# Kernel optimization log

Hardware: AMD Instinct MI355X
Metric: run time of the kernel (lower is better)

Reference implementation:

```python
import jax, jax.numpy as jnp
import numpy as np

T, D, E, DE = 50000, 128, 1600000, 3
EPS = 1e-5


def setup_inputs() -> dict:
    key = jax.random.key(0)
    ks = jax.random.split(key, 8)
    H = jax.random.normal(ks[0], (T, D), dtype=jnp.float32)
    edge_index = jax.random.randint(ks[1], (2, E), 0, T, dtype=jnp.int64)
    edge_attr = jax.random.normal(ks[2], (E, DE), dtype=jnp.float32)
    # phi: Linear(D+DE -> D), GELU, Linear(D -> D)
    s1 = 1.0 / np.sqrt(D + DE)
    s2 = 1.0 / np.sqrt(D)
    W1 = jax.random.uniform(ks[3], (D + DE, D), minval=-s1, maxval=s1, dtype=jnp.float32)
    b1 = jax.random.uniform(ks[4], (D,), minval=-s1, maxval=s1, dtype=jnp.float32)
    W2 = jax.random.uniform(ks[5], (D, D), minval=-s2, maxval=s2, dtype=jnp.float32)
    b2 = jax.random.uniform(ks[6], (D,), minval=-s2, maxval=s2, dtype=jnp.float32)
    gamma = jnp.ones((D,), dtype=jnp.float32)
    beta = jnp.zeros((D,), dtype=jnp.float32)
    return {"H": H, "edge_index": edge_index, "edge_attr": edge_attr,
            "W1": W1, "b1": b1, "W2": W2, "b2": b2, "gamma": gamma, "beta": beta}


def reference(H, edge_index, edge_attr, W1, b1, W2, b2, gamma, beta):
    src, dst = edge_index[0], edge_index[1]
    Hj = H[src]                                   # [E, D] gather
    feat = jnp.concatenate([Hj, edge_attr], axis=-1)  # [E, D+DE]
    h = jax.nn.gelu(feat @ W1 + b1, approximate=False)
    m = h @ W2 + b2                               # [E, D] messages
    agg = jax.ops.segment_sum(m, dst, num_segments=H.shape[0])  # scatter-add
    x = H + agg
    mu = jnp.mean(x, axis=-1, keepdims=True)
    var = jnp.mean((x - mu) ** 2, axis=-1, keepdims=True)
    return (x - mu) * jax.lax.rsqrt(var + EPS) * gamma + beta
```

## Files before the change

kernel.cpp:

```cpp
#include <hip/hip_runtime.h>
#include <hip/hip_bf16.h>

typedef unsigned short u16;
typedef unsigned int u32;
typedef __attribute__((ext_vector_type(8))) __bf16 bf16x8;
typedef __attribute__((ext_vector_type(4))) float f32x4;

#define NT 50000
#define NEDGE 1600000
#define GRID 512
#define NWV 8
#define TOTW 4096
#define NBIN 50176

__device__ __forceinline__ u16 f2bf(float f) {
  unsigned x = __float_as_uint(f);
  x += 0x7fffu + ((x >> 16) & 1u);
  return (u16)(x >> 16);
}

__device__ __forceinline__ int swz(int row, int col) {
  return (row << 7) + (col ^ ((row & 7) << 3));
}

__device__ __forceinline__ float gelu(float v) {
  float t = v * (0.797884561f + 0.0356774081f * v * v);
  return v * __builtin_amdgcn_rcpf(1.0f + __expf(-2.0f * t));
}

__device__ __forceinline__ void atomAddF32(float* p, float v) {
#if defined(__has_builtin)
#if __has_builtin(__builtin_amdgcn_global_atomic_fadd_f32)
  __builtin_amdgcn_global_atomic_fadd_f32((__attribute__((address_space(1))) float*)p, v);
  return;
#endif
#endif
  atomicAdd(p, v);
}


__global__ void prep_all(const float* __restrict__ H, u16* __restrict__ Hb,
                         const float* __restrict__ W1, const float* __restrict__ W2,
                         u16* __restrict__ wsw, const float* __restrict__ b1,
                         u16* __restrict__ wx, u32* __restrict__ cnt) {
  int bid = blockIdx.x, tid = threadIdx.x;
  if (bid < 3125) {
    int t = bid * 256 + tid;
    const float4* s = (const float4*)H + (long)t * 2;
    float4 a = s[0], c = s[1];
    int4 pk;
    pk.x = f2bf(a.x) | ((int)f2bf(a.y) << 16);
    pk.y = f2bf(a.z) | ((int)f2bf(a.w) << 16);
    pk.z = f2bf(c.x) | ((int)f2bf(c.y) << 16);
    pk.w = f2bf(c.z) | ((int)f2bf(c.w) << 16);
    ((int4*)Hb)[t] = pk;
  } else if (bid < 3253) {
    int t = (bid - 3125) * 256 + tid;
    int m = t >> 14;
    int p = t & 16383;
    int row = p >> 7;
    int colq = p & 127;
    int k = colq ^ ((row & 7) << 3);
    const float* W = m ? W2 : W1;
    wsw[t] = f2bf(W[k * 128 + row]);
  } else if (bid < 3257) {
    int t = (bid - 3253) * 256 + tid;
    int row = t >> 3, j = t & 7;
    float v = 0.f;
    if (j < 3) v = W1[(128 + j) * 128 + row];
    else if (j == 3) v = b1[row];
    wx[t] = f2bf(v);
  } else if (bid < 3453) {
    int t = (bid - 3257) * 256 + tid;
    if (t < NBIN) cnt[t] = 0;
  } else {
    if (tid < 16) ((int4*)(Hb + (long)NT * 128))[tid] = make_int4(0, 0, 0, 0);
  }
}

__global__ void copy_h(const float4* __restrict__ H, float4* __restrict__ out) {
  int t = blockIdx.x * 256 + threadIdx.x;
  out[t] = H[t];
}


__global__ void hist_g(const int* __restrict__ ei, u32* __restrict__ cnt) {
  int e = blockIdx.x * 256 + threadIdx.x;
  atomicAdd(&cnt[ei[NEDGE + e]], 1u);
}

__global__ void scan_blk(u32* __restrict__ cnt, u32* __restrict__ btot) {
  __shared__ u32 ls[1024];
  int tid = threadIdx.x;
  int bin = blockIdx.x * 1024 + tid;
  u32 c = cnt[bin];
  ls[tid] = c;
  __syncthreads();
  for (int o = 1; o < 1024; o <<= 1) {
    u32 t = (tid >= o) ? ls[tid - o] : 0u;
    __syncthreads();
    ls[tid] += t;
    __syncthreads();
  }
  cnt[bin] = ls[tid] - c;
  if (tid == 1023) btot[blockIdx.x] = ls[1023];
}

__global__ void scan_btot(u32* __restrict__ btot) {
  if (threadIdx.x == 0) {
    u32 run = 0;
    for (int i = 0; i < 49; ++i) { u32 t = btot[i]; btot[i] = run; run += t; }
  }
}

__global__ void fin_base(const u32* __restrict__ cnt, const u32* __restrict__ btot,
                         u32* __restrict__ base, u32* __restrict__ pos) {
  int bin = blockIdx.x * 256 + threadIdx.x;
  if (bin < NT) {
    u32 v = cnt[bin] + btot[bin >> 10];
    base[bin] = v;
    pos[bin] = v;
  }
  if (bin == NT) base[NT] = NEDGE;
}

__global__ void scatter_g(const int* __restrict__ ei, const float* __restrict__ ea,
                          u32* __restrict__ pos, uint2* __restrict__ rec) {
  int e = blockIdx.x * 256 + threadIdx.x;
  int d = ei[NEDGE + e];
  int s = ei[e];
  float e0 = ea[e * 3 + 0], e1 = ea[e * 3 + 1], e2 = ea[e * 3 + 2];
  u32 p = atomicAdd(&pos[d], 1u);
  rec[p] = make_uint2((u32)s | ((u32)f2bf(e0) << 16),
                      (u32)f2bf(e1) | ((u32)f2bf(e2) << 16));
}


__launch_bounds__(512, 2)
__global__ void msg_agg(const u16* __restrict__ Hb,
                        const u16* __restrict__ wsw,
                        const u16* __restrict__ wx,
                        const u32* __restrict__ base,
                        const uint2* __restrict__ rec,
                        u16* __restrict__ hsb) {
  __shared__ __align__(16) u16 lw1[16384];
  __shared__ __align__(16) u16 lw1x[128 * 8];

  const int tid = threadIdx.x;
  {
    const int4* g = (const int4*)wsw;
    int4* d1 = (int4*)lw1;
#pragma unroll
    for (int i = 0; i < 4; ++i) { int c = tid + i * 512; d1[c] = g[c]; }
  }
  if (tid < 128) ((int4*)lw1x)[tid] = ((const int4*)wx)[tid];
  __syncthreads();

  const int wv = tid >> 6, lane = tid & 63;
  const int l15 = lane & 15, l4 = lane >> 4;

  const int gid = blockIdx.x * NWV + wv;
  const int d0 = (int)(((long)gid * NT) / TOTW);
  const int d1i = (int)(((long)(gid + 1) * NT) / TOTW);
  const int nd = d1i - d0;

  for (int b = 0; b < nd; ++b) {
    const int start = (int)base[d0 + b];
    const int cnt = (int)base[d0 + b + 1] - start;

    float racc[8][4];
#pragma unroll
    for (int nt = 0; nt < 8; ++nt)
#pragma unroll
      for (int r = 0; r < 4; ++r) racc[nt][r] = 0.f;

    const int ntile = (cnt + 15) >> 4;
    uint2 r2c = make_uint2(0, 0);
    if (ntile > 0) {
      int i0 = (l15 < cnt) ? l15 : cnt - 1;
      r2c = rec[start + i0];
    }

    for (int t = 0; t < ntile; ++t) {
      int inx = (t + 1) * 16 + l15;
      if (inx >= cnt) inx = cnt - 1;
      uint2 r2n = rec[start + inx];

      const bool valid = (t * 16 + l15) < cnt;
      int src = valid ? (int)(r2c.x & 0xFFFFu) : NT;
      u32 x0 = 0u, x1 = 0u;
      if (l4 == 0 && valid) {
        x0 = (r2c.x >> 16) | (r2c.y << 16);
        x1 = (r2c.y >> 16) | 0x3F800000u;
      }
      int4 xbi = make_int4((int)x0, (int)x1, 0, 0);
      bf16x8 bfrx = *(bf16x8*)&xbi;

      bf16x8 bfc[4];
      {
        const u16* hr = Hb + (long)src * 128;
#pragma unroll
        for (int ks = 0; ks < 4; ++ks)
          bfc[ks] = *(const bf16x8*)(hr + ks * 32 + l4 * 8);
      }

#pragma unroll
      for (int nt = 0; nt < 8; ++nt) {
        bf16x8 afr[4];
#pragma unroll
        for (int ks = 0; ks < 4; ++ks)
          afr[ks] = *(const bf16x8*)&lw1[swz(nt * 16 + l15, ks * 32 + l4 * 8)];
        bf16x8 afrx = *(const bf16x8*)&lw1x[(nt * 16 + l15) * 8];
        f32x4 acc = (f32x4){0.f, 0.f, 0.f, 0.f};
#pragma unroll
        for (int ks = 0; ks < 4; ++ks)
          acc = __builtin_amdgcn_mfma_f32_16x16x32_bf16(bfc[ks], afr[ks], acc, 0, 0, 0);
        acc = __builtin_amdgcn_mfma_f32_16x16x32_bf16(bfrx, afrx, acc, 0, 0, 0);
#pragma unroll
        for (int r = 0; r < 4; ++r)
          racc[nt][r] += gelu(acc[r]);
      }
      r2c = r2n;
    }

    float sv[8];
#pragma unroll
    for (int nt = 0; nt < 8; ++nt) {
      float s = racc[nt][0] + racc[nt][1] + racc[nt][2] + racc[nt][3];
      s += __shfl_xor(s, 16);
      s += __shfl_xor(s, 32);
      sv[nt] = s;
    }
    float sa = (l4 == 0) ? sv[0] : (l4 == 1) ? sv[1] : (l4 == 2) ? sv[2] : sv[3];
    float sb = (l4 == 0) ? sv[4] : (l4 == 1) ? sv[5] : (l4 == 2) ? sv[6] : sv[7];
    u16* hrow = hsb + (long)(d0 + b) * 128;
    hrow[l4 * 16 + l15] = f2bf(sa);
    hrow[64 + l4 * 16 + l15] = f2bf(sb);
  }
}


__launch_bounds__(256)
__global__ void gemm_ln(const u16* __restrict__ hsb,
                        const float* __restrict__ H,
                        const float* __restrict__ b2,
                        const u16* __restrict__ wsw,
                        const u32* __restrict__ base,
                        const float* __restrict__ gamma,
                        const float* __restrict__ beta,
                        float* __restrict__ out) {
  __shared__ __align__(16) u16 lw2[16384];
  const int tid = threadIdx.x;
  {
    const int4* g = (const int4*)wsw + 2048;
    int4* d2 = (int4*)lw2;
#pragma unroll
    for (int i = 0; i < 8; ++i) { int c = tid + i * 256; d2[c] = g[c]; }
  }
  __syncthreads();

  const int wv = tid >> 6, lane = tid & 63;
  const int l15 = lane & 15, l4 = lane >> 4;
  const int r0 = (blockIdx.x * 4 + wv) * 16;

  bf16x8 ha[4];
#pragma unroll
  for (int ks = 0; ks < 4; ++ks)
    ha[ks] = *(const bf16x8*)(hsb + (long)(r0 + l15) * 128 + ks * 32 + l4 * 8);

  float cntr[4];
#pragma unroll
  for (int r = 0; r < 4; ++r) {
    int row = r0 + l4 * 4 + r;
    if (row > NT - 1) row = NT - 1;
    cntr[r] = (float)(base[row + 1] - base[row]);
  }

  float xv[8][4];
#pragma unroll
  for (int nt = 0; nt < 8; ++nt) {
    bf16x8 bfr2[4];
#pragma unroll
    for (int ks = 0; ks < 4; ++ks)
      bfr2[ks] = *(const bf16x8*)&lw2[swz(nt * 16 + l15, ks * 32 + l4 * 8)];
    float b2v = b2[nt * 16 + l15];
    f32x4 acc = (f32x4){0.f, 0.f, 0.f, 0.f};
#pragma unroll
    for (int ks = 0; ks < 4; ++ks)
      acc = __builtin_amdgcn_mfma_f32_16x16x32_bf16(ha[ks], bfr2[ks], acc, 0, 0, 0);
#pragma unroll
    for (int r = 0; r < 4; ++r) {
      int row = r0 + l4 * 4 + r;
      long o = (long)((row < NT) ? row : NT - 1) * 128 + nt * 16 + l15;
      xv[nt][r] = H[o] + acc[r] + cntr[r] * b2v;
    }
  }

  float mu[4], rs[4];
#pragma unroll
  for (int r = 0; r < 4; ++r) {
    float s = 0.f;
#pragma unroll
    for (int nt = 0; nt < 8; ++nt) s += xv[nt][r];
    s += __shfl_xor(s, 1); s += __shfl_xor(s, 2);
    s += __shfl_xor(s, 4); s += __shfl_xor(s, 8);
    mu[r] = s * (1.0f / 128.0f);
    float q = 0.f;
#pragma unroll
    for (int nt = 0; nt < 8; ++nt) {
      float d = xv[nt][r] - mu[r];
      q += d * d;
    }
    q += __shfl_xor(q, 1); q += __shfl_xor(q, 2);
    q += __shfl_xor(q, 4); q += __shfl_xor(q, 8);
    rs[r] = rsqrtf(q * (1.0f / 128.0f) + 1e-5f);
  }

#pragma unroll
  for (int nt = 0; nt < 8; ++nt) {
    int col = nt * 16 + l15;
    float g = gamma[col], bb = beta[col];
#pragma unroll
    for (int r = 0; r < 4; ++r) {
      int row = r0 + l4 * 4 + r;
      if (row < NT)
        out[(long)row * 128 + col] = (xv[nt][r] - mu[r]) * rs[r] * g + bb;
    }
  }
}


template <int BF16H>
__launch_bounds__(256, 1)
__global__ void msg_atomic(const float* __restrict__ H,
                           const u16* __restrict__ Hb,
                           const int* __restrict__ ei,
                           const float* __restrict__ ea,
                           const float* __restrict__ W1,
                           const float* __restrict__ b1,
                           const float* __restrict__ b2,
                           const u16* __restrict__ wsw,
                           float* __restrict__ out) {
  __shared__ __align__(16) u16 lw1[16384];
  __shared__ __align__(16) u16 lw2[16384];
  __shared__ __align__(16) u16 lh[4 * 2048];
  __shared__ __align__(16) float lep[5][128];

  const int tid = threadIdx.x;
  {
    const int4* g = (const int4*)wsw;
    int4* d1 = (int4*)lw1;
    int4* d2 = (int4*)lw2;
#pragma unroll
    for (int i = 0; i < 8; ++i) {
      int c = tid + i * 256;
      d1[c] = g[c];
      d2[c] = g[2048 + c];
    }
  }
  if (tid < 128) {
    lep[0][tid] = b1[tid];
    lep[1][tid] = W1[128 * 128 + tid];
    lep[2][tid] = W1[129 * 128 + tid];
    lep[3][tid] = W1[130 * 128 + tid];
    lep[4][tid] = b2[tid];
  }
  __syncthreads();

  const int wv = tid >> 6, lane = tid & 63;
  const int l15 = lane & 15, l4 = lane >> 4;
  u16* lhw = lh + wv * 2048;
  const int gwid = blockIdx.x * 4 + wv;

  for (int g = gwid; g < NEDGE / 16; g += 4096) {
    const int eb = g * 16;
    int src = ei[eb + l15];
    float ea0 = ea[(eb + l15) * 3 + 0], ea1 = ea[(eb + l15) * 3 + 1], ea2 = ea[(eb + l15) * 3 + 2];

    bf16x8 bfr[4];
    if (BF16H) {
      const u16* hr = Hb + (long)src * 128;
#pragma unroll
      for (int ks = 0; ks < 4; ++ks)
        bfr[ks] = *(const bf16x8*)(hr + ks * 32 + l4 * 8);
    } else {
      const float* hr = H + (long)src * 128;
#pragma unroll
      for (int ks = 0; ks < 4; ++ks) {
        float4 a = *(const float4*)(hr + ks * 32 + l4 * 8);
        float4 c = *(const float4*)(hr + ks * 32 + l4 * 8 + 4);
        int4 pk;
        pk.x = f2bf(a.x) | ((int)f2bf(a.y) << 16);
        pk.y = f2bf(a.z) | ((int)f2bf(a.w) << 16);
        pk.z = f2bf(c.x) | ((int)f2bf(c.y) << 16);
        pk.w = f2bf(c.z) | ((int)f2bf(c.w) << 16);
        bfr[ks] = *(bf16x8*)&pk;
      }
    }

#pragma unroll
    for (int nt = 0; nt < 8; ++nt) {
      bf16x8 afr[4];
#pragma unroll
      for (int ks = 0; ks < 4; ++ks)
        afr[ks] = *(const bf16x8*)&lw1[swz(nt * 16 + l15, ks * 32 + l4 * 8)];
      f32x4 acc = (f32x4){0.f, 0.f, 0.f, 0.f};
#pragma unroll
      for (int ks = 0; ks < 4; ++ks)
        acc = __builtin_amdgcn_mfma_f32_16x16x32_bf16(afr[ks], bfr[ks], acc, 0, 0, 0);
      f32x4 b1v = *(const f32x4*)&lep[0][nt * 16 + l4 * 4];
      f32x4 w0v = *(const f32x4*)&lep[1][nt * 16 + l4 * 4];
      f32x4 w1v = *(const f32x4*)&lep[2][nt * 16 + l4 * 4];
      f32x4 w2v = *(const f32x4*)&lep[3][nt * 16 + l4 * 4];
      float hv[4];
#pragma unroll
      for (int r = 0; r < 4; ++r) {
        float v = acc[r] + b1v[r] + ea0 * w0v[r] + ea1 * w1v[r] + ea2 * w2v[r];
        hv[r] = gelu(v);
      }
      int2 hp;
      hp.x = f2bf(hv[0]) | ((int)f2bf(hv[1]) << 16);
      hp.y = f2bf(hv[2]) | ((int)f2bf(hv[3]) << 16);
      *(int2*)&lhw[swz(l15, nt * 16 + l4 * 4)] = hp;
    }

    asm volatile("" ::: "memory");

    bf16x8 ha[4];
#pragma unroll
    for (int ks = 0; ks < 4; ++ks)
      ha[ks] = *(const bf16x8*)&lhw[swz(l15, ks * 32 + l4 * 8)];
    int drow[4];
#pragma unroll
    for (int r = 0; r < 4; ++r) drow[r] = ei[NEDGE + eb + l4 * 4 + r];

#pragma unroll
    for (int nt = 0; nt < 8; ++nt) {
      bf16x8 bfr2[4];
#pragma unroll
      for (int ks = 0; ks < 4; ++ks)
        bfr2[ks] = *(const bf16x8*)&lw2[swz(nt * 16 + l15, ks * 32 + l4 * 8)];
      float b2v = lep[4][nt * 16 + l15];
      f32x4 acc = (f32x4){0.f, 0.f, 0.f, 0.f};
#pragma unroll
      for (int ks = 0; ks < 4; ++ks)
        acc = __builtin_amdgcn_mfma_f32_16x16x32_bf16(ha[ks], bfr2[ks], acc, 0, 0, 0);
#pragma unroll
      for (int r = 0; r < 4; ++r)
        atomAddF32(out + (long)drow[r] * 128 + nt * 16 + l15, acc[r] + b2v);
    }
  }
}

__global__ void ln_rows(float* __restrict__ out, const float* __restrict__ gamma,
                        const float* __restrict__ beta) {
  int wave = threadIdx.x >> 6, lane = threadIdx.x & 63;
  int row = blockIdx.x * 4 + wave;
  float2 v = *(const float2*)(out + (long)row * 128 + lane * 2);
  float s = v.x + v.y;
#pragma unroll
  for (int off = 32; off; off >>= 1) s += __shfl_xor(s, off);
  float mu = s * (1.0f / 128.0f);
  float dx = v.x - mu, dy = v.y - mu;
  float q = dx * dx + dy * dy;
#pragma unroll
  for (int off = 32; off; off >>= 1) q += __shfl_xor(q, off);
  float rs = rsqrtf(q * (1.0f / 128.0f) + 1e-5f);
  float2 g = *(const float2*)(gamma + lane * 2);
  float2 b = *(const float2*)(beta + lane * 2);
  float2 o;
  o.x = dx * rs * g.x + b.x;
  o.y = dy * rs * g.y + b.y;
  *(float2*)(out + (long)row * 128 + lane * 2) = o;
}

extern "C" void kernel_launch(void* const* d_in, const int* in_sizes, int n_in,
                              void* d_out, int out_size, void* d_ws, size_t ws_size,
                              hipStream_t stream) {
  const float* H   = (const float*)d_in[0];
  const int* ei    = (const int*)d_in[1];
  const float* ea  = (const float*)d_in[2];
  const float* W1  = (const float*)d_in[3];
  const float* b1  = (const float*)d_in[4];
  const float* W2  = (const float*)d_in[5];
  const float* b2  = (const float*)d_in[6];
  const float* gam = (const float*)d_in[7];
  const float* bet = (const float*)d_in[8];
  float* out = (float*)d_out;

  char* ws = (char*)d_ws;
  u16* wsw   = (u16*)ws;
  u16* wx    = (u16*)(ws + 65536);
  u16* Hb    = (u16*)(ws + 67584);
  u32* cnt   = (u32*)(ws + 12867840);
  u32* base  = (u32*)(ws + 13068544);
  u32* pos   = (u32*)(ws + 13268560);
  u32* btot  = (u32*)(ws + 13468560);
  uint2* rec = (uint2*)(ws + 13468816);
  u16* hsb   = (u16*)(ws + 26268816);
  const size_t NEED_FULL = 39081104;
  const size_t NEED_HB = 12867840;

  if (ws_size >= NEED_FULL) {
    prep_all<<<3454, 256, 0, stream>>>(H, Hb, W1, W2, wsw, b1, wx, cnt);
    hist_g<<<6250, 256, 0, stream>>>(ei, cnt);
    scan_blk<<<49, 1024, 0, stream>>>(cnt, btot);
    scan_btot<<<1, 64, 0, stream>>>(btot);
    fin_base<<<196, 256, 0, stream>>>(cnt, btot, base, pos);
    scatter_g<<<6250, 256, 0, stream>>>(ei, ea, pos, rec);
    msg_agg<<<GRID, 512, 0, stream>>>(Hb, wsw, wx, base, rec, hsb);
    gemm_ln<<<782, 256, 0, stream>>>(hsb, H, b2, wsw, base, gam, bet, out);
  } else if (ws_size >= NEED_HB) {
    prep_all<<<3454, 256, 0, stream>>>(H, Hb, W1, W2, wsw, b1, wx, cnt);
    copy_h<<<6250, 256, 0, stream>>>((const float4*)H, (float4*)out);
    msg_atomic<1><<<1024, 256, 0, stream>>>(H, Hb, ei, ea, W1, b1, b2, wsw, out);
    ln_rows<<<12500, 256, 0, stream>>>(out, gam, bet);
  } else {
    copy_h<<<6250, 256, 0, stream>>>((const float4*)H, (float4*)out);
    msg_atomic<0><<<1024, 256, 0, stream>>>(H, Hb, ei, ea, W1, b1, b2, wsw, out);
    ln_rows<<<12500, 256, 0, stream>>>(out, gam, bet);
  }
}
```

Baseline: 359.5 us.

## Balance msg_agg by edge count, fold btot scan, cheaper GELU

Each msg_agg wave now binary-searches the CSR base array so it receives an equal share of edges instead of an equal share of destination nodes. This targets load imbalance from nodes with very different degrees. The change also merges the single-thread btot scan into fin_base (one fewer launch), zeroes the histogram with hipMemsetAsync instead of extra prep blocks, rewrites GELU using exp2 with prefolded constants, and loads A fragments per MFMA to reduce register pressure. Each block of fin_base now redoes a serial 49-element scan, and the per-wave binary search adds a startup cost.

```diff
diff --git a/kernel.cpp b/kernel.cpp
--- a/kernel.cpp
+++ b/kernel.cpp
@@ -24,8 +24,10 @@
 }
 
 __device__ __forceinline__ float gelu(float v) {
-  float t = v * (0.797884561f + 0.0356774081f * v * v);
-  return v * __builtin_amdgcn_rcpf(1.0f + __expf(-2.0f * t));
+  float u = v * v;
+  float arg = v * __builtin_fmaf(-0.1029434f, u, -2.3022082f);
+  float e = __builtin_amdgcn_exp2f(arg);
+  return v * __builtin_amdgcn_rcpf(1.0f + e);
 }
 
 __device__ __forceinline__ void atomAddF32(float* p, float v) {
@@ -42,7 +44,7 @@
 __global__ void prep_all(const float* __restrict__ H, u16* __restrict__ Hb,
                          const float* __restrict__ W1, const float* __restrict__ W2,
                          u16* __restrict__ wsw, const float* __restrict__ b1,
-                         u16* __restrict__ wx, u32* __restrict__ cnt) {
+                         u16* __restrict__ wx) {
   int bid = blockIdx.x, tid = threadIdx.x;
   if (bid < 3125) {
     int t = bid * 256 + tid;
@@ -70,9 +72,6 @@
     if (j < 3) v = W1[(128 + j) * 128 + row];
     else if (j == 3) v = b1[row];
     wx[t] = f2bf(v);
-  } else if (bid < 3453) {
-    int t = (bid - 3257) * 256 + tid;
-    if (t < NBIN) cnt[t] = 0;
   } else {
     if (tid < 16) ((int4*)(Hb + (long)NT * 128))[tid] = make_int4(0, 0, 0, 0);
   }
@@ -106,18 +105,18 @@
   if (tid == 1023) btot[blockIdx.x] = ls[1023];
 }
 
-__global__ void scan_btot(u32* __restrict__ btot) {
-  if (threadIdx.x == 0) {
-    u32 run = 0;
-    for (int i = 0; i < 49; ++i) { u32 t = btot[i]; btot[i] = run; run += t; }
-  }
-}
-
 __global__ void fin_base(const u32* __restrict__ cnt, const u32* __restrict__ btot,
                          u32* __restrict__ base, u32* __restrict__ pos) {
-  int bin = blockIdx.x * 256 + threadIdx.x;
+  __shared__ u32 bpre[49];
+  int tid = threadIdx.x;
+  if (tid == 0) {
+    u32 run = 0;
+    for (int i = 0; i < 49; ++i) { u32 t = btot[i]; bpre[i] = run; run += t; }
+  }
+  __syncthreads();
+  int bin = blockIdx.x * 256 + tid;
   if (bin < NT) {
-    u32 v = cnt[bin] + btot[bin >> 10];
+    u32 v = cnt[bin] + bpre[bin >> 10];
     base[bin] = v;
     pos[bin] = v;
   }
@@ -158,15 +157,20 @@
 
   const int wv = tid >> 6, lane = tid & 63;
   const int l15 = lane & 15, l4 = lane >> 4;
-
   const int gid = blockIdx.x * NWV + wv;
-  const int d0 = (int)(((long)gid * NT) / TOTW);
-  const int d1i = (int)(((long)(gid + 1) * NT) / TOTW);
-  const int nd = d1i - d0;
-
-  for (int b = 0; b < nd; ++b) {
-    const int start = (int)base[d0 + b];
-    const int cnt = (int)base[d0 + b + 1] - start;
+
+  const long t0 = ((long)gid * NEDGE) / TOTW;
+  const long t1 = ((long)(gid + 1) * NEDGE) / TOTW;
+  int lo = 0, hi = NT;
+  while (lo < hi) { int mid = (lo + hi) >> 1; if ((long)base[mid] < t0) lo = mid + 1; else hi = mid; }
+  const int d0 = lo;
+  hi = NT;
+  while (lo < hi) { int mid = (lo + hi) >> 1; if ((long)base[mid] < t1) lo = mid + 1; else hi = mid; }
+  const int d1i = lo;
+
+  for (int b = d0; b < d1i; ++b) {
+    const int start = (int)base[b];
+    const int cnt = (int)base[b + 1] - start;
 
     float racc[8][4];
 #pragma unroll
@@ -206,15 +210,13 @@
 
 #pragma unroll
       for (int nt = 0; nt < 8; ++nt) {
-        bf16x8 afr[4];
-#pragma unroll
-        for (int ks = 0; ks < 4; ++ks)
-          afr[ks] = *(const bf16x8*)&lw1[swz(nt * 16 + l15, ks * 32 + l4 * 8)];
         bf16x8 afrx = *(const bf16x8*)&lw1x[(nt * 16 + l15) * 8];
         f32x4 acc = (f32x4){0.f, 0.f, 0.f, 0.f};
 #pragma unroll
-        for (int ks = 0; ks < 4; ++ks)
-          acc = __builtin_amdgcn_mfma_f32_16x16x32_bf16(bfc[ks], afr[ks], acc, 0, 0, 0);
+        for (int ks = 0; ks < 4; ++ks) {
+          bf16x8 afr = *(const bf16x8*)&lw1[swz(nt * 16 + l15, ks * 32 + l4 * 8)];
+          acc = __builtin_amdgcn_mfma_f32_16x16x32_bf16(bfc[ks], afr, acc, 0, 0, 0);
+        }
         acc = __builtin_amdgcn_mfma_f32_16x16x32_bf16(bfrx, afrx, acc, 0, 0, 0);
 #pragma unroll
         for (int r = 0; r < 4; ++r)
@@ -233,7 +235,7 @@
     }
     float sa = (l4 == 0) ? sv[0] : (l4 == 1) ? sv[1] : (l4 == 2) ? sv[2] : sv[3];
     float sb = (l4 == 0) ? sv[4] : (l4 == 1) ? sv[5] : (l4 == 2) ? sv[6] : sv[7];
-    u16* hrow = hsb + (long)(d0 + b) * 128;
+    u16* hrow = hsb + (long)b * 128;
     hrow[l4 * 16 + l15] = f2bf(sa);
     hrow[64 + l4 * 16 + l15] = f2bf(sb);
   }
@@ -496,22 +498,22 @@
   u32* base  = (u32*)(ws + 13068544);
   u32* pos   = (u32*)(ws + 13268560);
   u32* btot  = (u32*)(ws + 13468560);
-  uint2* rec = (uint2*)(ws + 13468816);
-  u16* hsb   = (u16*)(ws + 26268816);
-  const size_t NEED_FULL = 39081104;
+  uint2* rec = (uint2*)(ws + 13468832);
+  u16* hsb   = (u16*)(ws + 26268832);
+  const size_t NEED_FULL = 39081120;
   const size_t NEED_HB = 12867840;
 
   if (ws_size >= NEED_FULL) {
-    prep_all<<<3454, 256, 0, stream>>>(H, Hb, W1, W2, wsw, b1, wx, cnt);
+    hipMemsetAsync(cnt, 0, NBIN * sizeof(u32), stream);
+    prep_all<<<3258, 256, 0, stream>>>(H, Hb, W1, W2, wsw, b1, wx);
     hist_g<<<6250, 256, 0, stream>>>(ei, cnt);
     scan_blk<<<49, 1024, 0, stream>>>(cnt, btot);
-    scan_btot<<<1, 64, 0, stream>>>(btot);
     fin_base<<<196, 256, 0, stream>>>(cnt, btot, base, pos);
     scatter_g<<<6250, 256, 0, stream>>>(ei, ea, pos, rec);
     msg_agg<<<GRID, 512, 0, stream>>>(Hb, wsw, wx, base, rec, hsb);
     gemm_ln<<<782, 256, 0, stream>>>(hsb, H, b2, wsw, base, gam, bet, out);
   } else if (ws_size >= NEED_HB) {
-    prep_all<<<3454, 256, 0, stream>>>(H, Hb, W1, W2, wsw, b1, wx, cnt);
+    prep_all<<<3258, 256, 0, stream>>>(H, Hb, W1, W2, wsw, b1, wx);
     copy_h<<<6250, 256, 0, stream>>>((const float4*)H, (float4*)out);
     msg_atomic<1><<<1024, 256, 0, stream>>>(H, Hb, ei, ea, W1, b1, b2, wsw, out);
     ln_rows<<<12500, 256, 0, stream>>>(out, gam, bet);
```

After: 536.2 us. 1.49x slower.
